# Kernel optimization log

Measured on AMD Instinct MI355X. Metric: run time of the kernel, lower is better.

The kernel has to match this reference:

```python
import jax, jax.numpy as jnp
import numpy as np
import math

INPUT_SIZE = 4096
NUM_NEURONS = 4096
ATTN_SIZE = 64
BATCH = 8192


def setup_inputs() -> dict:
    key = jax.random.key(0)
    ks = jax.random.split(key, 10)
    lim_in = 1.0 / math.sqrt(INPUT_SIZE)
    lim_a = 1.0 / math.sqrt(ATTN_SIZE)
    x = jax.random.normal(ks[0], (BATCH, INPUT_SIZE), dtype=jnp.float32)
    # attention linears (torch default uniform(-1/sqrt(fan_in), ...))
    Wq = jax.random.uniform(ks[1], (ATTN_SIZE, INPUT_SIZE), jnp.float32, -lim_in, lim_in)
    bq = jnp.zeros((ATTN_SIZE,), jnp.float32)
    Wk = jax.random.uniform(ks[2], (ATTN_SIZE, INPUT_SIZE), jnp.float32, -lim_in, lim_in)
    bk = jnp.zeros((ATTN_SIZE,), jnp.float32)
    Wv = jax.random.uniform(ks[3], (ATTN_SIZE, INPUT_SIZE), jnp.float32, -lim_in, lim_in)
    bv = jnp.zeros((ATTN_SIZE,), jnp.float32)
    Wo = jax.random.uniform(ks[4], (INPUT_SIZE, ATTN_SIZE), jnp.float32, -lim_a, lim_a)
    bo = jnp.zeros((INPUT_SIZE,), jnp.float32)
    # stacked single-weight neurons: weight ~ N(0,1)*0.01, bias 0
    Wn = jax.random.normal(ks[5], (NUM_NEURONS, INPUT_SIZE), jnp.float32) * 0.01
    bn = jnp.zeros((NUM_NEURONS,), jnp.float32)
    return {"x": x, "Wq": Wq, "bq": bq, "Wk": Wk, "bk": bk,
            "Wv": Wv, "bv": bv, "Wo": Wo, "bo": bo, "Wn": Wn, "bn": bn}


def reference(x, Wq, bq, Wk, bk, Wv, bv, Wo, bo, Wn, bn):
    scale = math.sqrt(ATTN_SIZE)
    # x is treated as a length-1 "sequence" of the full feature vector: [B, 1, S]
    q = x @ Wq.T + bq            # [B, A]
    k = x @ Wk.T + bk            # [B, A]
    v = x @ Wv.T + bv            # [B, A]
    # attention over a single token: softmax of a single score == 1, kept for fidelity
    scores = jnp.sum(q * k, axis=-1, keepdims=True) / scale      # [B, 1]
    attn_w = jax.nn.softmax(scores[:, :, None], axis=-1)          # [B, 1, 1] -> all ones
    attended = attn_w[:, 0, :] * v                                # [B, A] == v
    attn_out = attended @ Wo.T + bo                               # [B, S]
    h = attn_out + x                                              # residual
    # stacked single-weight neurons == one GEMM
    out = h @ Wn.T + bn                                           # [B, N]
    return jax.nn.relu(out)
```

## Files before the change

### kernel.cpp

```cpp
#include <hip/hip_runtime.h>
#include <stdint.h>


typedef unsigned short u16;
typedef float f32x4 __attribute__((ext_vector_type(4)));
typedef __bf16 bf16x8 __attribute__((ext_vector_type(8)));
typedef u16 u16x8 __attribute__((ext_vector_type(8)));

__device__ __forceinline__ float b2f(u16 u) {
  union { unsigned int i; float f; } x; x.i = ((unsigned int)u) << 16; return x.f;
}
__device__ __forceinline__ u16 f2b(float f) {
  union { float f; unsigned int i; } x; x.f = f;
  unsigned int r = x.i + 0x7FFFu + ((x.i >> 16) & 1u);
  return (u16)(r >> 16);
}

__device__ __forceinline__ void gl_lds16(const u16* g, u16* l) {
#if __has_builtin(__builtin_amdgcn_global_load_lds)
  __builtin_amdgcn_global_load_lds((__attribute__((address_space(1))) void*)g,
                                   (__attribute__((address_space(3))) void*)l, 16, 0, 0);
#else
  int lane = threadIdx.x & 63;
  *(u16x8*)(l + lane * 8) = *(const u16x8*)g;
#endif
}

__device__ __forceinline__ f32x4 mfma16(bf16x8 a, bf16x8 b, f32x4 c) {
  return __builtin_amdgcn_mfma_f32_16x16x32_bf16(a, b, c, 0, 0, 0);
}

#define XCH 4194304L
#define WNCH 2097152L
#define TOTG 6324224L
__global__ __launch_bounds__(256) void k_cvt(
    const float* __restrict__ x, const float* __restrict__ Wn,
    const float* __restrict__ Wv, const float* __restrict__ Wo,
    u16* __restrict__ xb, u16* __restrict__ Wnb, u16* __restrict__ Wvb,
    u16* __restrict__ WoT) {
  __shared__ __align__(16) u16 t[64 * 72];
  if (blockIdx.x < 64) {
    const int b = blockIdx.x;
    const int tid = threadIdx.x;
    {
      int k = tid >> 2, a0 = (tid & 3) * 16;
      const float* src = &Wo[(size_t)(b * 64 + k) * 64 + a0];
#pragma unroll
      for (int q = 0; q < 4; ++q) {
        f32x4 v = *(const f32x4*)&src[q * 4];
#pragma unroll
        for (int e = 0; e < 4; ++e) t[k * 72 + a0 + q * 4 + e] = f2b(v[e]);
      }
    }
    __syncthreads();
    {
      int a = tid >> 2, k0 = (tid & 3) * 16;
      u16x8 o0, o1;
#pragma unroll
      for (int j = 0; j < 8; ++j) o0[j] = t[(k0 + j) * 72 + a];
#pragma unroll
      for (int j = 0; j < 8; ++j) o1[j] = t[(k0 + 8 + j) * 72 + a];
      *(u16x8*)&WoT[(size_t)a * 4096 + b * 64 + k0] = o0;
      *(u16x8*)&WoT[(size_t)a * 4096 + b * 64 + k0 + 8] = o1;
    }
    return;
  }
  long i = (long)(blockIdx.x - 64) * 256 + threadIdx.x;
  const long stride = 2048L * 256;
  for (; i < TOTG; i += stride) {
    const float* src; u16* dst; long off;
    if (i < XCH) { src = x; dst = xb; off = i * 8; }
    else if (i < XCH + WNCH) { src = Wn; dst = Wnb; off = (i - XCH) * 8; }
    else { src = Wv; dst = Wvb; off = (i - XCH - WNCH) * 8; }
    f32x4 a = *(const f32x4*)&src[off];
    f32x4 b = *(const f32x4*)&src[off + 4];
    u16x8 o;
#pragma unroll
    for (int e = 0; e < 4; ++e) { o[e] = f2b(a[e]); o[4 + e] = f2b(b[e]); }
    *(u16x8*)&dst[off] = o;
  }
}

#define PBK 128
__device__ void gemm_n64(const u16* __restrict__ A, const u16* __restrict__ B,
                         u16* __restrict__ C, const float* __restrict__ bias,
                         long m0, u16* lA, u16* lB) {
  const int tid = threadIdx.x;
  const int w = tid >> 6, l = tid & 63;
  f32x4 acc[4];
#pragma unroll
  for (int nt = 0; nt < 4; ++nt) acc[nt] = (f32x4)(0.f);

  for (int k0 = 0; k0 < 4096; k0 += PBK) {
    __syncthreads();
#pragma unroll
    for (int i = 0; i < 4; ++i) {
      int row = w * 16 + i * 4 + (l >> 4);
      int p = (l & 15) ^ (i * 4 + (l >> 4));
      gl_lds16(A + (m0 + row) * (long)4096 + k0 + p * 8, lA + (w * 16 + i * 4) * PBK);
      gl_lds16(B + (long)row * 4096 + k0 + p * 8, lB + (w * 16 + i * 4) * PBK);
    }
    __syncthreads();
#pragma unroll
    for (int kk = 0; kk < 4; ++kk) {
      int slotA = ((kk * 4 + (l >> 4)) ^ (l & 15)) * 8;
      bf16x8 af = *(const bf16x8*)&lA[(w * 16 + (l & 15)) * PBK + slotA];
#pragma unroll
      for (int nt = 0; nt < 4; ++nt) {
        bf16x8 bf = *(const bf16x8*)&lB[(nt * 16 + (l & 15)) * PBK + slotA];
        acc[nt] = mfma16(af, bf, acc[nt]);
      }
    }
  }
#pragma unroll
  for (int nt = 0; nt < 4; ++nt) {
    int col = nt * 16 + (l & 15);
    float bb = bias ? bias[col] : 0.f;
#pragma unroll
    for (int r = 0; r < 4; ++r) {
      long row = m0 + w * 16 + (l >> 4) * 4 + r;
      C[row * 64 + col] = f2b(acc[nt][r] + bb);
    }
  }
}

__global__ __launch_bounds__(256, 2) void k_prep(
    const u16* __restrict__ xb, const u16* __restrict__ Wvb, const float* __restrict__ bv,
    const u16* __restrict__ Wnb, const u16* __restrict__ WoT,
    const float* __restrict__ bo, const float* __restrict__ bn,
    u16* __restrict__ V, u16* __restrict__ Wm, float* __restrict__ biasTot) {
  __shared__ __align__(16) u16 lA[64 * PBK];
  __shared__ __align__(16) u16 lB[64 * PBK];
  const int bid = blockIdx.x;
  if (bid < 128) {
    gemm_n64(xb, Wvb, V, bv, (long)bid * 64, lA, lB);
  } else if (bid < 192) {
    gemm_n64(Wnb, WoT, Wm, nullptr, (long)(bid - 128) * 64, lA, lB);
  } else {
    const int w = threadIdx.x >> 6, l = threadIdx.x & 63;
    const int n = (bid - 192) * 4 + w;
    float s = 0.f;
#pragma unroll
    for (int j = 0; j < 8; ++j) {
      int off = (j * 64 + l) * 8;
      u16x8 a = *(const u16x8*)&Wnb[(size_t)n * 4096 + off];
      f32x4 c0 = *(const f32x4*)&bo[off];
      f32x4 c1 = *(const f32x4*)&bo[off + 4];
#pragma unroll
      for (int e = 0; e < 4; ++e) s += b2f(a[e]) * c0[e] + b2f(a[4 + e]) * c1[e];
    }
#pragma unroll
    for (int o = 32; o > 0; o >>= 1) s += __shfl_xor(s, o, 64);
    if (l == 0) biasTot[n] = s + bn[n];
  }
}

__global__ __launch_bounds__(256, 2) void k_main(
    const u16* __restrict__ X, const u16* __restrict__ Wn,
    const u16* __restrict__ V, const u16* __restrict__ Wm,
    const float* __restrict__ biasTot, float* __restrict__ Out) {
  __shared__ __align__(16) u16 smem[2 * 128 * 64];
  u16* lA = smem;
  u16* lB = smem + 128 * 64;
  const int tid = threadIdx.x;
  const int w = tid >> 6, l = tid & 63;
  const int wRow = (w & 1) * 64, wCol = (w >> 1) * 64;
  const long mBase = (long)(blockIdx.x >> 5) * 128;
  const int nBase = (int)(blockIdx.x & 31) * 128;

  f32x4 acc[4][4];
#pragma unroll
  for (int mt = 0; mt < 4; ++mt)
#pragma unroll
    for (int nt = 0; nt < 4; ++nt) acc[mt][nt] = (f32x4)(0.f);

  const int srow = l >> 3;
  const int sp = ((l & 7) ^ srow) * 8;

  for (int kb = 0; kb < 65; ++kb) {
    const u16 *pA, *pB; long lda;
    if (kb < 64) { pA = X + (long)kb * 64; pB = Wn + (long)kb * 64; lda = 4096; }
    else         { pA = V;                 pB = Wm;                 lda = 64;  }
    __syncthreads();
#pragma unroll
    for (int i = 0; i < 4; ++i) {
      int row = w * 32 + i * 8 + srow;
      gl_lds16(pA + (mBase + row) * lda + sp, lA + (w * 32 + i * 8) * 64);
      gl_lds16(pB + (long)(nBase + row) * lda + sp, lB + (w * 32 + i * 8) * 64);
    }
    __syncthreads();
#pragma unroll
    for (int kk = 0; kk < 2; ++kk) {
      int slot = ((kk * 4 + (l >> 4)) ^ (l & 7)) * 8;
      bf16x8 af[4], bfr[4];
#pragma unroll
      for (int mt = 0; mt < 4; ++mt)
        af[mt] = *(const bf16x8*)&lA[(wRow + mt * 16 + (l & 15)) * 64 + slot];
#pragma unroll
      for (int nt = 0; nt < 4; ++nt)
        bfr[nt] = *(const bf16x8*)&lB[(wCol + nt * 16 + (l & 15)) * 64 + slot];
#pragma unroll
      for (int mt = 0; mt < 4; ++mt)
#pragma unroll
        for (int nt = 0; nt < 4; ++nt) acc[mt][nt] = mfma16(af[mt], bfr[nt], acc[mt][nt]);
    }
  }

  __syncthreads();
  float* eb = ((float*)smem) + w * 1024;
#pragma unroll
  for (int mt = 0; mt < 4; ++mt) {
#pragma unroll
    for (int nt = 0; nt < 4; ++nt) {
      float bt = biasTot[nBase + wCol + nt * 16 + (l & 15)];
#pragma unroll
      for (int r = 0; r < 4; ++r) {
        float val = acc[mt][nt][r] + bt;
        eb[((l >> 4) * 4 + r) * 64 + nt * 16 + (l & 15)] = fmaxf(val, 0.f);
      }
    }
    int rr = l >> 2, c0 = (l & 3) * 16;
    long grow = mBase + wRow + mt * 16 + rr;
    int gcol = nBase + wCol + c0;
    f32x4 o0 = *(const f32x4*)&eb[rr * 64 + c0];
    f32x4 o1 = *(const f32x4*)&eb[rr * 64 + c0 + 4];
    f32x4 o2 = *(const f32x4*)&eb[rr * 64 + c0 + 8];
    f32x4 o3 = *(const f32x4*)&eb[rr * 64 + c0 + 12];
    *(f32x4*)&Out[grow * 4096 + gcol] = o0;
    *(f32x4*)&Out[grow * 4096 + gcol + 4] = o1;
    *(f32x4*)&Out[grow * 4096 + gcol + 8] = o2;
    *(f32x4*)&Out[grow * 4096 + gcol + 12] = o3;
  }
}

extern "C" void kernel_launch(void* const* d_in, const int* in_sizes, int n_in,
                              void* d_out, int out_size, void* d_ws, size_t ws_size,
                              hipStream_t stream) {
  const float* x  = (const float*)d_in[0];
  const float* Wv = (const float*)d_in[5];
  const float* bv = (const float*)d_in[6];
  const float* Wo = (const float*)d_in[7];
  const float* bo = (const float*)d_in[8];
  const float* Wn = (const float*)d_in[9];
  const float* bn = (const float*)d_in[10];
  float* out = (float*)d_out;

  char* ws = (char*)d_ws;
  u16* xb  = (u16*)ws;
  u16* Wnb = (u16*)(ws + (64L << 20));
  u16* Wvb = (u16*)(ws + (96L << 20));
  u16* WoT = (u16*)(ws + (96L << 20) + (512 << 10));
  u16* V   = (u16*)(ws + (97L << 20));
  u16* Wm  = (u16*)(ws + (98L << 20));
  float* biasTot = (float*)(ws + (98L << 20) + (512 << 10));

  k_cvt<<<dim3(2112), dim3(256), 0, stream>>>(x, Wn, Wv, Wo, xb, Wnb, Wvb, WoT);
  k_prep<<<dim3(1216), dim3(256), 0, stream>>>(xb, Wvb, bv, Wnb, WoT, bo, bn, V, Wm, biasTot);
  k_main<<<dim3(2048), dim3(256), 0, stream>>>(xb, Wnb, V, Wm, biasTot, out);
}
```

Measured before the change: 608.7 us.

## Enlarge main GEMM block tile to 256x128 with 128x64 per-wave tiles

The main GEMM block tile grows from 128x128 to 256x128, and each wave now computes a 128x64 sub-tile with 32 accumulator fragments, halving the grid. This raises arithmetic intensity per LDS load and per global fetch of B, at the cost of higher register pressure (128 accumulator floats per thread) and larger LDS use, which may reduce occupancy under launch_bounds(256,2). The change also adds s_setprio around the MFMA block and hoists the bias loads out of the epilogue loop.

After: 589.2 us. -3.2%, faster.

```diff
diff --git a/kernel.cpp b/kernel.cpp
--- a/kernel.cpp
+++ b/kernel.cpp
@@ -159,69 +159,81 @@
     const u16* __restrict__ X, const u16* __restrict__ Wn,
     const u16* __restrict__ V, const u16* __restrict__ Wm,
     const float* __restrict__ biasTot, float* __restrict__ Out) {
-  __shared__ __align__(16) u16 smem[2 * 128 * 64];
-  u16* lA = smem;
-  u16* lB = smem + 128 * 64;
+  __shared__ __align__(16) u16 smem[24576];
   const int tid = threadIdx.x;
   const int w = tid >> 6, l = tid & 63;
-  const int wRow = (w & 1) * 64, wCol = (w >> 1) * 64;
-  const long mBase = (long)(blockIdx.x >> 5) * 128;
-  const int nBase = (int)(blockIdx.x & 31) * 128;
-
-  f32x4 acc[4][4];
-#pragma unroll
-  for (int mt = 0; mt < 4; ++mt)
+  const int wm = w >> 1, wn = w & 1;
+  const long mBase = (long)(blockIdx.x >> 5) * 256;
+  const int  nBase = (int)(blockIdx.x & 31) * 128;
+
+  const int rsub = w * 8 + (l >> 3);
+  const int swe  = ((l & 7) ^ (l >> 3)) * 8;
+  const int ldsS = w * 512;
+
+  const int frow = l & 15, fsl = l >> 4, fx = l & 7;
+  const int sl0 = (fsl ^ fx) * 8;
+  const int sl1 = ((4 + fsl) ^ fx) * 8;
+  const int aB = wm * 8192 + frow * 64;
+  const int bB = 16384 + wn * 4096 + frow * 64;
+
+  f32x4 acc[8][4];
+#pragma unroll
+  for (int mt = 0; mt < 8; ++mt)
 #pragma unroll
     for (int nt = 0; nt < 4; ++nt) acc[mt][nt] = (f32x4)(0.f);
 
-  const int srow = l >> 3;
-  const int sp = ((l & 7) ^ srow) * 8;
-
   for (int kb = 0; kb < 65; ++kb) {
-    const u16 *pA, *pB; long lda;
-    if (kb < 64) { pA = X + (long)kb * 64; pB = Wn + (long)kb * 64; lda = 4096; }
-    else         { pA = V;                 pB = Wm;                 lda = 64;  }
-    __syncthreads();
-#pragma unroll
-    for (int i = 0; i < 4; ++i) {
-      int row = w * 32 + i * 8 + srow;
-      gl_lds16(pA + (mBase + row) * lda + sp, lA + (w * 32 + i * 8) * 64);
-      gl_lds16(pB + (long)(nBase + row) * lda + sp, lB + (w * 32 + i * 8) * 64);
-    }
+    const u16 *pA, *pB; long lda, ko;
+    if (kb < 64) { pA = X; pB = Wn; lda = 4096; ko = (long)kb * 64; }
+    else         { pA = V; pB = Wm; lda = 64;   ko = 0; }
+    __syncthreads();
+#pragma unroll
+    for (int op = 0; op < 8; ++op)
+      gl_lds16(pA + (mBase + op * 32 + rsub) * lda + ko + swe,
+               smem + op * 2048 + ldsS);
+#pragma unroll
+    for (int op = 0; op < 4; ++op)
+      gl_lds16(pB + ((long)nBase + op * 32 + rsub) * lda + ko + swe,
+               smem + 16384 + op * 2048 + ldsS);
     __syncthreads();
 #pragma unroll
     for (int kk = 0; kk < 2; ++kk) {
-      int slot = ((kk * 4 + (l >> 4)) ^ (l & 7)) * 8;
-      bf16x8 af[4], bfr[4];
-#pragma unroll
-      for (int mt = 0; mt < 4; ++mt)
-        af[mt] = *(const bf16x8*)&lA[(wRow + mt * 16 + (l & 15)) * 64 + slot];
+      const int sl = kk ? sl1 : sl0;
+      bf16x8 af[8], bf[4];
+#pragma unroll
+      for (int mt = 0; mt < 8; ++mt)
+        af[mt] = *(const bf16x8*)&smem[aB + mt * 1024 + sl];
 #pragma unroll
       for (int nt = 0; nt < 4; ++nt)
-        bfr[nt] = *(const bf16x8*)&lB[(wCol + nt * 16 + (l & 15)) * 64 + slot];
-#pragma unroll
-      for (int mt = 0; mt < 4; ++mt)
-#pragma unroll
-        for (int nt = 0; nt < 4; ++nt) acc[mt][nt] = mfma16(af[mt], bfr[nt], acc[mt][nt]);
+        bf[nt] = *(const bf16x8*)&smem[bB + nt * 1024 + sl];
+      __builtin_amdgcn_s_setprio(1);
+#pragma unroll
+      for (int mt = 0; mt < 8; ++mt)
+#pragma unroll
+        for (int nt = 0; nt < 4; ++nt)
+          acc[mt][nt] = mfma16(af[mt], bf[nt], acc[mt][nt]);
+      __builtin_amdgcn_s_setprio(0);
     }
   }
 
   __syncthreads();
   float* eb = ((float*)smem) + w * 1024;
-#pragma unroll
-  for (int mt = 0; mt < 4; ++mt) {
+  float bt[4];
+#pragma unroll
+  for (int nt = 0; nt < 4; ++nt) bt[nt] = biasTot[nBase + wn * 64 + nt * 16 + frow];
+#pragma unroll
+  for (int mt = 0; mt < 8; ++mt) {
 #pragma unroll
     for (int nt = 0; nt < 4; ++nt) {
-      float bt = biasTot[nBase + wCol + nt * 16 + (l & 15)];
 #pragma unroll
       for (int r = 0; r < 4; ++r) {
-        float val = acc[mt][nt][r] + bt;
-        eb[((l >> 4) * 4 + r) * 64 + nt * 16 + (l & 15)] = fmaxf(val, 0.f);
+        float val = acc[mt][nt][r] + bt[nt];
+        eb[(fsl * 4 + r) * 64 + nt * 16 + frow] = fmaxf(val, 0.f);
       }
     }
     int rr = l >> 2, c0 = (l & 3) * 16;
-    long grow = mBase + wRow + mt * 16 + rr;
-    int gcol = nBase + wCol + c0;
+    long grow = mBase + wm * 128 + mt * 16 + rr;
+    int gcol = nBase + wn * 64 + c0;
     f32x4 o0 = *(const f32x4*)&eb[rr * 64 + c0];
     f32x4 o1 = *(const f32x4*)&eb[rr * 64 + c0 + 4];
     f32x4 o2 = *(const f32x4*)&eb[rr * 64 + c0 + 8];
@@ -256,5 +268,5 @@
 
   k_cvt<<<dim3(2112), dim3(256), 0, stream>>>(x, Wn, Wv, Wo, xb, Wnb, Wvb, WoT);
   k_prep<<<dim3(1216), dim3(256), 0, stream>>>(xb, Wvb, bv, Wnb, WoT, bo, bn, V, Wm, biasTot);
-  k_main<<<dim3(2048), dim3(256), 0, stream>>>(xb, Wnb, V, Wm, biasTot, out);
-}
+  k_main<<<dim3(1024), dim3(256), 0, stream>>>(xb, Wnb, V, Wm, biasTot, out);
+}
```
